# Performance work log

Hardware: AMD Instinct MI355X
Metric: run time of the kernel (lower is better)

The kernel has to match this reference:

```python
import jax, jax.numpy as jnp
import numpy as np
from jax import lax

L, E, H, V, B, S = 25, 64, 8, 30000, 1000, 512


def setup_inputs() -> dict:
    key = jax.random.key(0)
    ks = jax.random.split(key, 24)
    p = lambda k, shape: (jax.random.normal(k, shape) * 0.1).astype(jnp.float32)
    inp = {
        "x": jax.random.randint(ks[0], (B, S), 0, V),
        "embedding": p(ks[1], (V, E)),
        # layer 0 (input dim = E)
        "W_xz0": p(ks[2], (E, H)), "W_hz0": p(ks[3], (H, H)), "b_z0": p(ks[4], (H,)),
        "W_xr0": p(ks[5], (E, H)), "W_hr0": p(ks[6], (H, H)), "b_r0": p(ks[7], (H,)),
        "W_xH0": p(ks[8], (E, H)), "W_rH0": p(ks[9], (H, H)), "b_H0": p(ks[10], (H,)),
        # layers 1..L-1 stacked (input dim = H)
        "W_xz": p(ks[11], (L - 1, H, H)), "W_hz": p(ks[12], (L - 1, H, H)), "b_z": p(ks[13], (L - 1, H)),
        "W_xr": p(ks[14], (L - 1, H, H)), "W_hr": p(ks[15], (L - 1, H, H)), "b_r": p(ks[16], (L - 1, H)),
        "W_xH": p(ks[17], (L - 1, H, H)), "W_rH": p(ks[18], (L - 1, H, H)), "b_H": p(ks[19], (L - 1, H)),
        "W_hy": p(ks[20], (H, 1)), "b_y": p(ks[21], (1,)),
    }
    return inp


def _cell(x_t, h, Wxz, Whz, bz, Wxr, Whr, br, WxH, WrH, bH):
    z = jax.nn.sigmoid(x_t @ Wxz + h @ Whz + bz)
    r = jax.nn.sigmoid(x_t @ Wxr + h @ Whr + br)
    Hc = jnp.tanh(x_t @ WxH + (h * r) @ WrH + bH)
    return h * (1.0 - z) + z * Hc


def reference(x, embedding, W_xz0, W_hz0, b_z0, W_xr0, W_hr0, b_r0, W_xH0, W_rH0, b_H0,
              W_xz, W_hz, b_z, W_xr, W_hr, b_r, W_xH, W_rH, b_H, W_hy, b_y):
    emb = embedding[x]                     # [B, S, E]
    bsz = x.shape[0]
    h0 = jnp.zeros((L, bsz, H), dtype=embedding.dtype)

    def time_step(h_all, x_t):            # h_all: [L, B, H]; x_t: [B, E]
        h_new0 = _cell(x_t, h_all[0], W_xz0, W_hz0, b_z0, W_xr0, W_hr0, b_r0, W_xH0, W_rH0, b_H0)

        def layer_step(inp_t, ws):
            Wxz, Whz, bz, Wxr, Whr, br, WxH, WrH, bH, h_prev = ws
            h_new = _cell(inp_t, h_prev, Wxz, Whz, bz, Wxr, Whr, br, WxH, WrH, bH)
            return h_new, h_new

        _, h_rest = lax.scan(layer_step, h_new0,
                             (W_xz, W_hz, b_z, W_xr, W_hr, b_r, W_xH, W_rH, b_H, h_all[1:]))
        return jnp.concatenate([h_new0[None], h_rest], axis=0), None

    h_last, _ = lax.scan(time_step, h0, jnp.swapaxes(emb, 0, 1))  # scan over S
    logits = h_last[-1] @ W_hy + b_y       # [B, 1]
    return logits.squeeze(-1), h_last
```

## Files before the change

kernel.cpp:

```cpp
#include <hip/hip_runtime.h>
#include <hip/hip_bf16.h>
#include <stdint.h>

#define L_ 25
#define E_ 64
#define H_ 8
#define B_ 1000
#define S_ 512
#define GQ 2
#define NCELL (L_ * GQ)
#define TPBR (NCELL * 8)
#define NSUPER (S_ / 2 + L_ - 1)
#define HS 12
#define XG 20

typedef float v2f __attribute__((ext_vector_type(2)));
typedef float v4f __attribute__((ext_vector_type(4)));

#define PIN(x) asm volatile("" : "+v"(x))

__device__ __forceinline__ v2f pkfma(v2f a, v2f b, v2f c) {
  v2f d;
  asm("v_pk_fma_f32 %0, %1, %2, %3" : "=v"(d) : "v"(a), "v"(b), "v"(c));
  return d;
}
__device__ __forceinline__ v2f vlo(v4f v) { return __builtin_shufflevector(v, v, 0, 1); }
__device__ __forceinline__ v2f vhi(v4f v) { return __builtin_shufflevector(v, v, 2, 3); }
__device__ __forceinline__ v2f mk2(float a, float b) { v2f r; r.x = a; r.y = b; return r; }

__device__ __forceinline__ float ulo(uint32_t u) { return __uint_as_float(u << 16); }
__device__ __forceinline__ float uhi(uint32_t u) { return __uint_as_float(u & 0xffff0000u); }

__device__ __forceinline__ float toF(float v) { return v; }
__device__ __forceinline__ float toF(__hip_bfloat16 v) { return __bfloat162float(v); }
__device__ __forceinline__ void stP(float* p, float v) { *p = v; }
__device__ __forceinline__ void stP(__hip_bfloat16* p, float v) { *p = __float2bfloat16(v); }

__device__ __forceinline__ void load8f(const __hip_bfloat16* p, float* o) {
  const uint4 v = *(const uint4*)p;
  o[0] = ulo(v.x); o[1] = uhi(v.x); o[2] = ulo(v.y); o[3] = uhi(v.y);
  o[4] = ulo(v.z); o[5] = uhi(v.z); o[6] = ulo(v.w); o[7] = uhi(v.w);
}
__device__ __forceinline__ void load8f(const float* p, float* o) {
  const float4 a = ((const float4*)p)[0];
  const float4 b = ((const float4*)p)[1];
  o[0] = a.x; o[1] = a.y; o[2] = a.z; o[3] = a.w;
  o[4] = b.x; o[5] = b.y; o[6] = b.z; o[7] = b.w;
}

__device__ __forceinline__ void st4(float* p, float a, float b, float c, float d) {
  float4 v; v.x = a; v.y = b; v.z = c; v.w = d;
  *(float4*)p = v;
}
__device__ __forceinline__ void st4(__hip_bfloat16* p, float a, float b, float c, float d) {
  __hip_bfloat16 t[4] = {__float2bfloat16(a), __float2bfloat16(b),
                         __float2bfloat16(c), __float2bfloat16(d)};
  *(ushort4*)p = *(ushort4*)t;
}

__device__ __forceinline__ float sigmo(float x) {
  return __builtin_amdgcn_rcpf(1.f + __expf(-x));
}
__device__ __forceinline__ float tanh_(float x) {
  const float e = __expf(-2.f * x);
  return fmaf(2.f, __builtin_amdgcn_rcpf(1.f + e), -1.f);
}

__global__ void gru_detect(const unsigned short* __restrict__ u16, int* __restrict__ flag) {
  const int i = threadIdx.x;
  float m = 0.f;
#pragma unroll
  for (int k = 0; k < 4; ++k) {
    const uint32_t u = u16[i * 4 + k];
    float v = fabsf(__uint_as_float(u << 16));
    if (!(v < 1e30f)) v = 1e30f;
    m = fmaxf(m, v);
  }
#pragma unroll
  for (int off = 32; off; off >>= 1) m = fmaxf(m, __shfl_down(m, off, 64));
  if (i == 0) *flag = (m > 2.0f) ? 0 : 1;
}

template <typename T, typename PT>
__global__ __launch_bounds__(256, 4) void gru_pre(
    const int* __restrict__ flag, int want,
    const int* __restrict__ x, const T* __restrict__ emb,
    const T* __restrict__ Wz, const T* __restrict__ Wr,
    const T* __restrict__ Wh, PT* __restrict__ pre) {
  if (*flag != want) return;
  __shared__ __align__(16) float WL[64 * 24];
  __shared__ __align__(16) float TB[4][24 * 65];
  for (int idx = threadIdx.x; idx < 64 * 24; idx += 256) {
    const int k = idx / 24, c = idx - k * 24;
    const T* src = (c < 8) ? Wz : ((c < 16) ? Wr : Wh);
    WL[idx] = toF(src[k * 8 + (c & 7)]);
  }
  __syncthreads();

  const int tok = blockIdx.x * 256 + threadIdx.x;
  const int t = x[tok];

  v2f acc[12];
#pragma unroll
  for (int q = 0; q < 12; ++q) acc[q] = mk2(0.f, 0.f);

  for (int kb = 0; kb < 8; ++kb) {
    float e[8];
    load8f(emb + (size_t)t * E_ + kb * 8, e);
#pragma unroll
    for (int k8 = 0; k8 < 8; ++k8) {
      const v4f* wr = (const v4f*)(WL + (kb * 8 + k8) * 24);
      const v2f ee = mk2(e[k8], e[k8]);
#pragma unroll
      for (int q = 0; q < 6; ++q) {
        const v4f w4 = wr[q];
        acc[2 * q]     = pkfma(ee, vlo(w4), acc[2 * q]);
        acc[2 * q + 1] = pkfma(ee, vhi(w4), acc[2 * q + 1]);
      }
    }
  }

  const int wid = threadIdx.x >> 6, lane = threadIdx.x & 63;
  float* tb = &TB[wid][0];
#pragma unroll
  for (int q = 0; q < 12; ++q) {
    tb[(2 * q) * 65 + lane] = acc[q].x;
    tb[(2 * q + 1) * 65 + lane] = acc[q].y;
  }
  asm volatile("s_waitcnt lgkmcnt(0)" ::: "memory");
  __builtin_amdgcn_wave_barrier();

  PT* ob = pre + (size_t)(blockIdx.x * 256 + wid * 64) * 24;
#pragma unroll
  for (int it = 0; it < 6; ++it) {
    const int F0 = it * 256 + lane * 4;
    float o[4];
#pragma unroll
    for (int e2 = 0; e2 < 4; ++e2) {
      const int F = F0 + e2;
      const int tk = F / 24;
      const int c = F - tk * 24;
      o[e2] = tb[c * 65 + tk];
    }
    st4(ob + F0, o[0], o[1], o[2], o[3]);
  }
}

template <typename T, typename PT>
__global__ __launch_bounds__(TPBR, 4) void gru_rec(
    const int* __restrict__ flag, int want,
    const PT* __restrict__ pre,
    const T* __restrict__ Whz0, const T* __restrict__ bz0,
    const T* __restrict__ Whr0, const T* __restrict__ br0,
    const T* __restrict__ WrH0, const T* __restrict__ bH0,
    const T* __restrict__ Wxz, const T* __restrict__ Whz,
    const T* __restrict__ bz, const T* __restrict__ Wxr,
    const T* __restrict__ Whr, const T* __restrict__ br,
    const T* __restrict__ WxH, const T* __restrict__ WrH,
    const T* __restrict__ bH, const T* __restrict__ Why,
    const T* __restrict__ by, T* __restrict__ out) {
  if (*flag != want) return;
  __shared__ __align__(16) float hsh[NCELL * HS];
  __shared__ __align__(16) float hrsh[NCELL * HS];
  __shared__ __align__(16) float xbuf[2 * NCELL * XG];

  const int tid = threadIdx.x;
  const int gi = tid >> 3;
  const int j = tid & 7;
  const int l = gi >> 1;
  const int g = gi & 1;
  const int b = blockIdx.x * GQ + g;

  for (int i = tid; i < NCELL * HS; i += TPBR) { hsh[i] = 0.f; hrsh[i] = 0.f; }
  for (int i = tid; i < 2 * NCELL * XG; i += TPBR) xbuf[i] = 0.f;

  v2f wxz2[4], whz2[4], wxr2[4], whr2[4], wxh2[4], wrh2[4];
  v2f bz2, br2, bh2;
  if (l == 0) {
#pragma unroll
    for (int q = 0; q < 4; ++q) {
      whz2[q] = mk2(toF(Whz0[(2 * q) * 8 + j]), toF(Whz0[(2 * q + 1) * 8 + j]));
      whr2[q] = mk2(toF(Whr0[(2 * q) * 8 + j]), toF(Whr0[(2 * q + 1) * 8 + j]));
      wrh2[q] = mk2(toF(WrH0[(2 * q) * 8 + j]), toF(WrH0[(2 * q + 1) * 8 + j]));
      wxz2[q] = mk2(0.f, 0.f); wxr2[q] = mk2(0.f, 0.f); wxh2[q] = mk2(0.f, 0.f);
    }
    bz2 = mk2(toF(bz0[j]), 0.f);
    br2 = mk2(toF(br0[j]), 0.f);
    bh2 = mk2(toF(bH0[j]), 0.f);
  } else {
    const int base = (l - 1) * 64;
#pragma unroll
    for (int q = 0; q < 4; ++q) {
      wxz2[q] = mk2(toF(Wxz[base + (2 * q) * 8 + j]), toF(Wxz[base + (2 * q + 1) * 8 + j]));
      whz2[q] = mk2(toF(Whz[base + (2 * q) * 8 + j]), toF(Whz[base + (2 * q + 1) * 8 + j]));
      wxr2[q] = mk2(toF(Wxr[base + (2 * q) * 8 + j]), toF(Wxr[base + (2 * q + 1) * 8 + j]));
      whr2[q] = mk2(toF(Whr[base + (2 * q) * 8 + j]), toF(Whr[base + (2 * q + 1) * 8 + j]));
      wxh2[q] = mk2(toF(WxH[base + (2 * q) * 8 + j]), toF(WxH[base + (2 * q + 1) * 8 + j]));
      wrh2[q] = mk2(toF(WrH[base + (2 * q) * 8 + j]), toF(WrH[base + (2 * q + 1) * 8 + j]));
    }
    bz2 = mk2(toF(bz[(l - 1) * 8 + j]), 0.f);
    br2 = mk2(toF(br[(l - 1) * 8 + j]), 0.f);
    bh2 = mk2(toF(bH[(l - 1) * 8 + j]), 0.f);
  }
#pragma unroll
  for (int q = 0; q < 4; ++q) {
    PIN(wxz2[q]); PIN(whz2[q]); PIN(wxr2[q]); PIN(whr2[q]); PIN(wxh2[q]); PIN(wrh2[q]);
  }
  PIN(bz2); PIN(br2); PIN(bh2);

  const PT* ppr = pre + (size_t)b * (S_ * 24) + j;
  float cz0 = 0.f, cr0 = 0.f, ch0 = 0.f, cz1 = 0.f, cr1 = 0.f, ch1 = 0.f;
  if (l == 0) {
    cz0 = toF(ppr[0]);  cr0 = toF(ppr[8]);  ch0 = toF(ppr[16]);
    cz1 = toF(ppr[24]); cr1 = toF(ppr[32]); ch1 = toF(ppr[40]);
  }

  float* hgw = hsh + gi * HS;
  float* hrg = hrsh + gi * HS;
  float* hgwj = hgw + j;
  float* hrgj = hrg + j;
  const int gp = (gi >= GQ) ? (gi - GQ) * XG : 0;
  const float* xpe = xbuf + NCELL * XG + gp;
  const float* xpo = xbuf + gp;
  float* xce = xbuf + gi * XG;
  float* xco = xbuf + NCELL * XG + gi * XG;

  float hown = 0.f;

  __syncthreads();

  for (int s = 0; s < NSUPER; ++s) {
    const unsigned rel = (unsigned)(s - l);
    if (rel < (unsigned)(S_ / 2)) {
      const float* xp = (s & 1) ? xpo : xpe;
      float* xc = (s & 1) ? xco : xce;

      const v4f h01 = ((const v4f*)hgw)[0];
      const v4f h23 = ((const v4f*)hgw)[1];
      const v4f xa0 = ((const v4f*)xp)[0];
      const v4f xb0 = ((const v4f*)xp)[1];
      const v4f xa1 = ((const v4f*)xp)[2];
      const v4f xb1 = ((const v4f*)xp)[3];

      float pz0 = 0.f, pr0 = 0.f, ph0 = 0.f, pz1 = 0.f, pr1 = 0.f, ph1 = 0.f;
      const bool pf = (l == 0) && (rel + 1u < (unsigned)(S_ / 2));
      if (pf) {
        const PT* pn = ppr + (rel + 1) * 48;
        pz0 = toF(pn[0]);  pr0 = toF(pn[8]);  ph0 = toF(pn[16]);
        pz1 = toF(pn[24]); pr1 = toF(pn[32]); ph1 = toF(pn[40]);
      }

      v2f arh = pkfma(vlo(h01), whr2[0], mk2(0.f, 0.f));
      arh = pkfma(vhi(h01), whr2[1], arh);
      arh = pkfma(vlo(h23), whr2[2], arh);
      arh = pkfma(vhi(h23), whr2[3], arh);
      v2f azh = pkfma(vlo(h01), whz2[0], mk2(0.f, 0.f));
      azh = pkfma(vhi(h01), whz2[1], azh);
      azh = pkfma(vlo(h23), whz2[2], azh);
      azh = pkfma(vhi(h23), whz2[3], azh);

      v2f arp = pkfma(vlo(xa0), wxr2[0], br2);
      arp = pkfma(vhi(xa0), wxr2[1], arp);
      arp = pkfma(vlo(xb0), wxr2[2], arp);
      arp = pkfma(vhi(xb0), wxr2[3], arp);
      v2f azp = pkfma(vlo(xa0), wxz2[0], bz2);
      azp = pkfma(vhi(xa0), wxz2[1], azp);
      azp = pkfma(vlo(xb0), wxz2[2], azp);
      azp = pkfma(vhi(xb0), wxz2[3], azp);
      v2f ahp = pkfma(vlo(xa0), wxh2[0], bh2);
      ahp = pkfma(vhi(xa0), wxh2[1], ahp);
      ahp = pkfma(vlo(xb0), wxh2[2], ahp);
      ahp = pkfma(vhi(xb0), wxh2[3], ahp);

      v2f arp1 = pkfma(vlo(xa1), wxr2[0], br2);
      arp1 = pkfma(vhi(xa1), wxr2[1], arp1);
      arp1 = pkfma(vlo(xb1), wxr2[2], arp1);
      arp1 = pkfma(vhi(xb1), wxr2[3], arp1);
      v2f azp1 = pkfma(vlo(xa1), wxz2[0], bz2);
      azp1 = pkfma(vhi(xa1), wxz2[1], azp1);
      azp1 = pkfma(vlo(xb1), wxz2[2], azp1);
      azp1 = pkfma(vhi(xb1), wxz2[3], azp1);
      v2f ahp1 = pkfma(vlo(xa1), wxh2[0], bh2);
      ahp1 = pkfma(vhi(xa1), wxh2[1], ahp1);
      ahp1 = pkfma(vlo(xb1), wxh2[2], ahp1);
      ahp1 = pkfma(vhi(xb1), wxh2[3], ahp1);

      const float ar0 = (arp.x + arp.y) + (arh.x + arh.y) + cr0;
      const float rA = sigmo(ar0);
      *hrgj = hown * rA;
      __builtin_amdgcn_wave_barrier();

      const v4f r01 = ((const v4f*)hrg)[0];
      const v4f r23 = ((const v4f*)hrg)[1];
      const float az0 = (azp.x + azp.y) + (azh.x + azh.y) + cz0;
      const float zA = sigmo(az0);
      ahp = pkfma(vlo(r01), wrh2[0], ahp);
      ahp = pkfma(vhi(r01), wrh2[1], ahp);
      ahp = pkfma(vlo(r23), wrh2[2], ahp);
      ahp = pkfma(vhi(r23), wrh2[3], ahp);
      const float ah0 = ahp.x + ahp.y + ch0;
      const float hn0 = fmaf(zA, tanh_(ah0) - hown, hown);
      *hgwj = hn0;
      xc[j] = hn0;
      __builtin_amdgcn_wave_barrier();

      const v4f g01 = ((const v4f*)hgw)[0];
      const v4f g23 = ((const v4f*)hgw)[1];
      arp1 = pkfma(vlo(g01), whr2[0], arp1);
      arp1 = pkfma(vhi(g01), whr2[1], arp1);
      arp1 = pkfma(vlo(g23), whr2[2], arp1);
      arp1 = pkfma(vhi(g23), whr2[3], arp1);
      azp1 = pkfma(vlo(g01), whz2[0], azp1);
      azp1 = pkfma(vhi(g01), whz2[1], azp1);
      azp1 = pkfma(vlo(g23), whz2[2], azp1);
      azp1 = pkfma(vhi(g23), whz2[3], azp1);
      const float ar1 = arp1.x + arp1.y + cr1;
      const float rB = sigmo(ar1);
      *hrgj = hn0 * rB;
      __builtin_amdgcn_wave_barrier();

      const v4f q01 = ((const v4f*)hrg)[0];
      const v4f q23 = ((const v4f*)hrg)[1];
      const float az1 = azp1.x + azp1.y + cz1;
      const float zB = sigmo(az1);
      ahp1 = pkfma(vlo(q01), wrh2[0], ahp1);
      ahp1 = pkfma(vhi(q01), wrh2[1], ahp1);
      ahp1 = pkfma(vlo(q23), wrh2[2], ahp1);
      ahp1 = pkfma(vhi(q23), wrh2[3], ahp1);
      const float ah1 = ahp1.x + ahp1.y + ch1;
      const float hn1 = fmaf(zB, tanh_(ah1) - hn0, hn0);
      *hgwj = hn1;
      xc[8 + j] = hn1;
      hown = hn1;
      if (pf) { cz0 = pz0; cr0 = pr0; ch0 = ph0; cz1 = pz1; cr1 = pr1; ch1 = ph1; }
    }
    __syncthreads();
  }

  stP(out + B_ + (l * B_ + b) * H_ + j, hown);
  if (l == L_ - 1 && j == 0) {
    float ssum = toF(by[0]);
#pragma unroll
    for (int k = 0; k < 8; ++k) ssum = fmaf(hgw[k], toF(Why[k]), ssum);
    stP(out + b, ssum);
  }
}

template <typename T, typename PT>
static void launch_mode(const int* flag, int want, void* const* d_in, PT* pre,
                        T* out, hipStream_t stream) {
  const int* x = (const int*)d_in[0];
  const T* emb = (const T*)d_in[1];
  const T* Wxz0 = (const T*)d_in[2];
  const T* Whz0 = (const T*)d_in[3];
  const T* bz0 = (const T*)d_in[4];
  const T* Wxr0 = (const T*)d_in[5];
  const T* Whr0 = (const T*)d_in[6];
  const T* br0 = (const T*)d_in[7];
  const T* WxH0 = (const T*)d_in[8];
  const T* WrH0 = (const T*)d_in[9];
  const T* bH0 = (const T*)d_in[10];
  const T* Wxz = (const T*)d_in[11];
  const T* Whz = (const T*)d_in[12];
  const T* bz = (const T*)d_in[13];
  const T* Wxr = (const T*)d_in[14];
  const T* Whr = (const T*)d_in[15];
  const T* br = (const T*)d_in[16];
  const T* WxH = (const T*)d_in[17];
  const T* WrH = (const T*)d_in[18];
  const T* bH = (const T*)d_in[19];
  const T* Why = (const T*)d_in[20];
  const T* by = (const T*)d_in[21];

  gru_pre<T, PT><<<B_ * S_ / 256, 256, 0, stream>>>(flag, want, x, emb,
                                                    Wxz0, Wxr0, WxH0, pre);
  gru_rec<T, PT><<<B_ / GQ, TPBR, 0, stream>>>(
      flag, want, pre, Whz0, bz0, Whr0, br0, WrH0, bH0, Wxz, Whz, bz, Wxr, Whr,
      br, WxH, WrH, bH, Why, by, out);
}

extern "C" void kernel_launch(void* const* d_in, const int* in_sizes, int n_in,
                              void* d_out, int out_size, void* d_ws, size_t ws_size,
                              hipStream_t stream) {
  int* flag = (int*)d_ws;
  char* preMem = (char*)d_ws + 256;
  const size_t needF = (size_t)B_ * S_ * 24 * sizeof(float) + 256;

  gru_detect<<<1, 64, 0, stream>>>((const unsigned short*)d_in[1], flag);

  if (ws_size >= needF) {
    float* pre = (float*)preMem;
    launch_mode<float, float>(flag, 0, d_in, pre, (float*)d_out, stream);
    launch_mode<__hip_bfloat16, float>(flag, 1, d_in, pre, (__hip_bfloat16*)d_out, stream);
  } else {
    __hip_bfloat16* pre = (__hip_bfloat16*)preMem;
    launch_mode<float, __hip_bfloat16>(flag, 0, d_in, pre, (float*)d_out, stream);
    launch_mode<__hip_bfloat16, __hip_bfloat16>(flag, 1, d_in, pre, (__hip_bfloat16*)d_out, stream);
  }
}
```

Baseline: 416.7 us.

## Fuse dtype detection into kernels, pack z/r gate math, widen batch per block

Drops the separate detect kernel and the four flag-gated launches. Each kernel now detects the dtype in-block and dispatches to a templated body, leaving two launches. The recurrence packs the z and r gate weights into interleaved pairs so a single op_sel-based packed FMA chain computes both gates together, and the pre-projection layout is interleaved to match. GQ goes from 2 to 4, so each block handles four batch rows with 800 threads and 250 blocks, which raises per-block parallelism but reduces block count and may pressure registers.

```diff
diff --git a/kernel.cpp b/kernel.cpp
--- a/kernel.cpp
+++ b/kernel.cpp
@@ -7,7 +7,7 @@
 #define H_ 8
 #define B_ 1000
 #define S_ 512
-#define GQ 2
+#define GQ 4
 #define NCELL (L_ * GQ)
 #define TPBR (NCELL * 8)
 #define NSUPER (S_ / 2 + L_ - 1)
@@ -24,9 +24,42 @@
   asm("v_pk_fma_f32 %0, %1, %2, %3" : "=v"(d) : "v"(a), "v"(b), "v"(c));
   return d;
 }
+__device__ __forceinline__ v2f pkfma_l(v2f a, v2f b, v2f c) {
+  v2f d;
+  asm("v_pk_fma_f32 %0, %1, %2, %3 op_sel:[0,0,0] op_sel_hi:[0,1,1]"
+      : "=v"(d) : "v"(a), "v"(b), "v"(c));
+  return d;
+}
+__device__ __forceinline__ v2f pkfma_h(v2f a, v2f b, v2f c) {
+  v2f d;
+  asm("v_pk_fma_f32 %0, %1, %2, %3 op_sel:[1,0,0] op_sel_hi:[1,1,1]"
+      : "=v"(d) : "v"(a), "v"(b), "v"(c));
+  return d;
+}
+__device__ __forceinline__ v2f pkadd(v2f a, v2f b) {
+  v2f d;
+  asm("v_pk_add_f32 %0, %1, %2" : "=v"(d) : "v"(a), "v"(b));
+  return d;
+}
 __device__ __forceinline__ v2f vlo(v4f v) { return __builtin_shufflevector(v, v, 0, 1); }
 __device__ __forceinline__ v2f vhi(v4f v) { return __builtin_shufflevector(v, v, 2, 3); }
 __device__ __forceinline__ v2f mk2(float a, float b) { v2f r; r.x = a; r.y = b; return r; }
+
+#define CHAIN8(acc, ma, mb, w)            \
+  acc = pkfma_l(vlo(ma), w[0], acc);      \
+  acc = pkfma_h(vlo(ma), w[1], acc);      \
+  acc = pkfma_l(vhi(ma), w[2], acc);      \
+  acc = pkfma_h(vhi(ma), w[3], acc);      \
+  acc = pkfma_l(vlo(mb), w[4], acc);      \
+  acc = pkfma_h(vlo(mb), w[5], acc);      \
+  acc = pkfma_l(vhi(mb), w[6], acc);      \
+  acc = pkfma_h(vhi(mb), w[7], acc);
+
+#define CHAIN4P(acc, ma, mb, w)           \
+  acc = pkfma(vlo(ma), w[0], acc);        \
+  acc = pkfma(vhi(ma), w[1], acc);        \
+  acc = pkfma(vlo(mb), w[2], acc);        \
+  acc = pkfma(vhi(mb), w[3], acc);
 
 __device__ __forceinline__ float ulo(uint32_t u) { return __uint_as_float(u << 16); }
 __device__ __forceinline__ float uhi(uint32_t u) { return __uint_as_float(u & 0xffff0000u); }
@@ -35,6 +68,12 @@
 __device__ __forceinline__ float toF(__hip_bfloat16 v) { return __bfloat162float(v); }
 __device__ __forceinline__ void stP(float* p, float v) { *p = v; }
 __device__ __forceinline__ void stP(__hip_bfloat16* p, float v) { *p = __float2bfloat16(v); }
+
+__device__ __forceinline__ v2f loadC2(const float* p) { return *(const v2f*)p; }
+__device__ __forceinline__ v2f loadC2(const __hip_bfloat16* p) {
+  const uint32_t u = *(const uint32_t*)p;
+  return mk2(ulo(u), uhi(u));
+}
 
 __device__ __forceinline__ void load8f(const __hip_bfloat16* p, float* o) {
   const uint4 v = *(const uint4*)p;
@@ -66,38 +105,45 @@
   return fmaf(2.f, __builtin_amdgcn_rcpf(1.f + e), -1.f);
 }
 
-__global__ void gru_detect(const unsigned short* __restrict__ u16, int* __restrict__ flag) {
-  const int i = threadIdx.x;
-  float m = 0.f;
-#pragma unroll
-  for (int k = 0; k < 4; ++k) {
-    const uint32_t u = u16[i * 4 + k];
-    float v = fabsf(__uint_as_float(u << 16));
-    if (!(v < 1e30f)) v = 1e30f;
-    m = fmaxf(m, v);
-  }
-#pragma unroll
-  for (int off = 32; off; off >>= 1) m = fmaxf(m, __shfl_down(m, off, 64));
-  if (i == 0) *flag = (m > 2.0f) ? 0 : 1;
+__device__ __forceinline__ void detect64(const unsigned short* __restrict__ u,
+                                         int tid, float* fl) {
+  if (tid < 64) {
+    float m = 0.f;
+#pragma unroll
+    for (int k = 0; k < 4; ++k) {
+      const uint32_t q = u[tid * 4 + k];
+      float v = fabsf(__uint_as_float(q << 16));
+      if (!(v < 1e30f)) v = 1e30f;
+      m = fmaxf(m, v);
+    }
+#pragma unroll
+    for (int off = 32; off; off >>= 1) m = fmaxf(m, __shfl_down(m, off, 64));
+    if (tid == 0) *fl = (m > 2.0f) ? 0.f : 1.f;
+  }
 }
 
 template <typename T, typename PT>
-__global__ __launch_bounds__(256, 4) void gru_pre(
-    const int* __restrict__ flag, int want,
-    const int* __restrict__ x, const T* __restrict__ emb,
-    const T* __restrict__ Wz, const T* __restrict__ Wr,
-    const T* __restrict__ Wh, PT* __restrict__ pre) {
-  if (*flag != want) return;
-  __shared__ __align__(16) float WL[64 * 24];
-  __shared__ __align__(16) float TB[4][24 * 65];
-  for (int idx = threadIdx.x; idx < 64 * 24; idx += 256) {
+__device__ __forceinline__ void pre_body(
+    const int* __restrict__ x, const void* __restrict__ embv,
+    const void* __restrict__ Wzv, const void* __restrict__ Wrv,
+    const void* __restrict__ Whv, PT* __restrict__ pre,
+    float* WL, float* TBb) {
+  const T* emb = (const T*)embv;
+  const T* Wz = (const T*)Wzv;
+  const T* Wr = (const T*)Wrv;
+  const T* Wh = (const T*)Whv;
+  const int tid = threadIdx.x;
+
+  for (int idx = tid; idx < 64 * 24; idx += 256) {
     const int k = idx / 24, c = idx - k * 24;
-    const T* src = (c < 8) ? Wz : ((c < 16) ? Wr : Wh);
-    WL[idx] = toF(src[k * 8 + (c & 7)]);
+    float w;
+    if (c < 16) w = toF(((c & 1) ? Wr : Wz)[k * 8 + (c >> 1)]);
+    else        w = toF(Wh[k * 8 + (c - 16)]);
+    WL[idx] = w;
   }
   __syncthreads();
 
-  const int tok = blockIdx.x * 256 + threadIdx.x;
+  const int tok = blockIdx.x * 256 + tid;
   const int t = x[tok];
 
   v2f acc[12];
@@ -120,8 +166,8 @@
     }
   }
 
-  const int wid = threadIdx.x >> 6, lane = threadIdx.x & 63;
-  float* tb = &TB[wid][0];
+  const int wid = tid >> 6, lane = tid & 63;
+  float* tb = TBb + wid * (24 * 65);
 #pragma unroll
   for (int q = 0; q < 12; ++q) {
     tb[(2 * q) * 65 + lane] = acc[q].x;
@@ -146,73 +192,95 @@
   }
 }
 
+template <typename PT>
+__global__ __launch_bounds__(256, 4) void gru_pre(
+    const int* __restrict__ x, const void* __restrict__ emb,
+    const void* __restrict__ Wz, const void* __restrict__ Wr,
+    const void* __restrict__ Wh, PT* __restrict__ pre) {
+  __shared__ __align__(16) float WL[64 * 24];
+  __shared__ __align__(16) float TB[4][24 * 65];
+  __shared__ float fl;
+  detect64((const unsigned short*)emb, threadIdx.x, &fl);
+  __syncthreads();
+  if (fl != 0.f) pre_body<__hip_bfloat16, PT>(x, emb, Wz, Wr, Wh, pre, WL, &TB[0][0]);
+  else           pre_body<float, PT>(x, emb, Wz, Wr, Wh, pre, WL, &TB[0][0]);
+}
+
 template <typename T, typename PT>
-__global__ __launch_bounds__(TPBR, 4) void gru_rec(
-    const int* __restrict__ flag, int want,
+__device__ __forceinline__ void rec_body(
     const PT* __restrict__ pre,
-    const T* __restrict__ Whz0, const T* __restrict__ bz0,
-    const T* __restrict__ Whr0, const T* __restrict__ br0,
-    const T* __restrict__ WrH0, const T* __restrict__ bH0,
-    const T* __restrict__ Wxz, const T* __restrict__ Whz,
-    const T* __restrict__ bz, const T* __restrict__ Wxr,
-    const T* __restrict__ Whr, const T* __restrict__ br,
-    const T* __restrict__ WxH, const T* __restrict__ WrH,
-    const T* __restrict__ bH, const T* __restrict__ Why,
-    const T* __restrict__ by, T* __restrict__ out) {
-  if (*flag != want) return;
-  __shared__ __align__(16) float hsh[NCELL * HS];
-  __shared__ __align__(16) float hrsh[NCELL * HS];
-  __shared__ __align__(16) float xbuf[2 * NCELL * XG];
+    const void* __restrict__ Whz0v, const void* __restrict__ bz0v,
+    const void* __restrict__ Whr0v, const void* __restrict__ br0v,
+    const void* __restrict__ WrH0v, const void* __restrict__ bH0v,
+    const void* __restrict__ Wxzv, const void* __restrict__ Whzv,
+    const void* __restrict__ bzv, const void* __restrict__ Wxrv,
+    const void* __restrict__ Whrv, const void* __restrict__ brv,
+    const void* __restrict__ WxHv, const void* __restrict__ WrHv,
+    const void* __restrict__ bHv, const void* __restrict__ Whyv,
+    const void* __restrict__ byv, void* __restrict__ outv,
+    float* hsh, float* hrsh, float* xbuf) {
+  const T* Whz0 = (const T*)Whz0v; const T* bz0 = (const T*)bz0v;
+  const T* Whr0 = (const T*)Whr0v; const T* br0 = (const T*)br0v;
+  const T* WrH0 = (const T*)WrH0v; const T* bH0 = (const T*)bH0v;
+  const T* Wxz = (const T*)Wxzv;   const T* Whz = (const T*)Whzv;
+  const T* bz = (const T*)bzv;     const T* Wxr = (const T*)Wxrv;
+  const T* Whr = (const T*)Whrv;   const T* br = (const T*)brv;
+  const T* WxH = (const T*)WxHv;   const T* WrH = (const T*)WrHv;
+  const T* bH = (const T*)bHv;     const T* Why = (const T*)Whyv;
+  const T* by = (const T*)byv;     T* out = (T*)outv;
 
   const int tid = threadIdx.x;
   const int gi = tid >> 3;
   const int j = tid & 7;
-  const int l = gi >> 1;
-  const int g = gi & 1;
+  const int l = gi >> 2;
+  const int g = gi & 3;
   const int b = blockIdx.x * GQ + g;
 
   for (int i = tid; i < NCELL * HS; i += TPBR) { hsh[i] = 0.f; hrsh[i] = 0.f; }
   for (int i = tid; i < 2 * NCELL * XG; i += TPBR) xbuf[i] = 0.f;
 
-  v2f wxz2[4], whz2[4], wxr2[4], whr2[4], wxh2[4], wrh2[4];
-  v2f bz2, br2, bh2;
+  v2f wzrx[8], wzrh[8], wxh2[4], wrh2[4], bzr;
+  float vbh;
   if (l == 0) {
 #pragma unroll
+    for (int k = 0; k < 8; ++k) {
+      wzrh[k] = mk2(toF(Whz0[k * 8 + j]), toF(Whr0[k * 8 + j]));
+      wzrx[k] = mk2(0.f, 0.f);
+    }
+#pragma unroll
     for (int q = 0; q < 4; ++q) {
-      whz2[q] = mk2(toF(Whz0[(2 * q) * 8 + j]), toF(Whz0[(2 * q + 1) * 8 + j]));
-      whr2[q] = mk2(toF(Whr0[(2 * q) * 8 + j]), toF(Whr0[(2 * q + 1) * 8 + j]));
       wrh2[q] = mk2(toF(WrH0[(2 * q) * 8 + j]), toF(WrH0[(2 * q + 1) * 8 + j]));
-      wxz2[q] = mk2(0.f, 0.f); wxr2[q] = mk2(0.f, 0.f); wxh2[q] = mk2(0.f, 0.f);
-    }
-    bz2 = mk2(toF(bz0[j]), 0.f);
-    br2 = mk2(toF(br0[j]), 0.f);
-    bh2 = mk2(toF(bH0[j]), 0.f);
+      wxh2[q] = mk2(0.f, 0.f);
+    }
+    bzr = mk2(toF(bz0[j]), toF(br0[j]));
+    vbh = toF(bH0[j]);
   } else {
     const int base = (l - 1) * 64;
 #pragma unroll
+    for (int k = 0; k < 8; ++k) {
+      wzrx[k] = mk2(toF(Wxz[base + k * 8 + j]), toF(Wxr[base + k * 8 + j]));
+      wzrh[k] = mk2(toF(Whz[base + k * 8 + j]), toF(Whr[base + k * 8 + j]));
+    }
+#pragma unroll
     for (int q = 0; q < 4; ++q) {
-      wxz2[q] = mk2(toF(Wxz[base + (2 * q) * 8 + j]), toF(Wxz[base + (2 * q + 1) * 8 + j]));
-      whz2[q] = mk2(toF(Whz[base + (2 * q) * 8 + j]), toF(Whz[base + (2 * q + 1) * 8 + j]));
-      wxr2[q] = mk2(toF(Wxr[base + (2 * q) * 8 + j]), toF(Wxr[base + (2 * q + 1) * 8 + j]));
-      whr2[q] = mk2(toF(Whr[base + (2 * q) * 8 + j]), toF(Whr[base + (2 * q + 1) * 8 + j]));
       wxh2[q] = mk2(toF(WxH[base + (2 * q) * 8 + j]), toF(WxH[base + (2 * q + 1) * 8 + j]));
       wrh2[q] = mk2(toF(WrH[base + (2 * q) * 8 + j]), toF(WrH[base + (2 * q + 1) * 8 + j]));
     }
-    bz2 = mk2(toF(bz[(l - 1) * 8 + j]), 0.f);
-    br2 = mk2(toF(br[(l - 1) * 8 + j]), 0.f);
-    bh2 = mk2(toF(bH[(l - 1) * 8 + j]), 0.f);
-  }
-#pragma unroll
-  for (int q = 0; q < 4; ++q) {
-    PIN(wxz2[q]); PIN(whz2[q]); PIN(wxr2[q]); PIN(whr2[q]); PIN(wxh2[q]); PIN(wrh2[q]);
-  }
-  PIN(bz2); PIN(br2); PIN(bh2);
-
-  const PT* ppr = pre + (size_t)b * (S_ * 24) + j;
-  float cz0 = 0.f, cr0 = 0.f, ch0 = 0.f, cz1 = 0.f, cr1 = 0.f, ch1 = 0.f;
+    bzr = mk2(toF(bz[(l - 1) * 8 + j]), toF(br[(l - 1) * 8 + j]));
+    vbh = toF(bH[(l - 1) * 8 + j]);
+  }
+#pragma unroll
+  for (int k = 0; k < 8; ++k) { PIN(wzrx[k]); PIN(wzrh[k]); }
+#pragma unroll
+  for (int q = 0; q < 4; ++q) { PIN(wxh2[q]); PIN(wrh2[q]); }
+  PIN(bzr); PIN(vbh);
+
+  const PT* ppr = pre + (size_t)b * (S_ * 24);
+  v2f czrA = mk2(0.f, 0.f), czrB = mk2(0.f, 0.f);
+  float chA = 0.f, chB = 0.f;
   if (l == 0) {
-    cz0 = toF(ppr[0]);  cr0 = toF(ppr[8]);  ch0 = toF(ppr[16]);
-    cz1 = toF(ppr[24]); cr1 = toF(ppr[32]); ch1 = toF(ppr[40]);
+    czrA = loadC2(ppr + 2 * j);      chA = toF(ppr[16 + j]);
+    czrB = loadC2(ppr + 24 + 2 * j); chB = toF(ppr[24 + 16 + j]);
   }
 
   float* hgw = hsh + gi * HS;
@@ -242,97 +310,60 @@
       const v4f xa1 = ((const v4f*)xp)[2];
       const v4f xb1 = ((const v4f*)xp)[3];
 
-      float pz0 = 0.f, pr0 = 0.f, ph0 = 0.f, pz1 = 0.f, pr1 = 0.f, ph1 = 0.f;
+      v2f nzrA = mk2(0.f, 0.f), nzrB = mk2(0.f, 0.f);
+      float nhA = 0.f, nhB = 0.f;
       const bool pf = (l == 0) && (rel + 1u < (unsigned)(S_ / 2));
       if (pf) {
-        const PT* pn = ppr + (rel + 1) * 48;
-        pz0 = toF(pn[0]);  pr0 = toF(pn[8]);  ph0 = toF(pn[16]);
-        pz1 = toF(pn[24]); pr1 = toF(pn[32]); ph1 = toF(pn[40]);
+        const PT* pn = ppr + (2 * rel + 2) * 24;
+        nzrA = loadC2(pn + 2 * j);      nhA = toF(pn[16 + j]);
+        nzrB = loadC2(pn + 24 + 2 * j); nhB = toF(pn[24 + 16 + j]);
       }
 
-      v2f arh = pkfma(vlo(h01), whr2[0], mk2(0.f, 0.f));
-      arh = pkfma(vhi(h01), whr2[1], arh);
-      arh = pkfma(vlo(h23), whr2[2], arh);
-      arh = pkfma(vhi(h23), whr2[3], arh);
-      v2f azh = pkfma(vlo(h01), whz2[0], mk2(0.f, 0.f));
-      azh = pkfma(vhi(h01), whz2[1], azh);
-      azh = pkfma(vlo(h23), whz2[2], azh);
-      azh = pkfma(vhi(h23), whz2[3], azh);
-
-      v2f arp = pkfma(vlo(xa0), wxr2[0], br2);
-      arp = pkfma(vhi(xa0), wxr2[1], arp);
-      arp = pkfma(vlo(xb0), wxr2[2], arp);
-      arp = pkfma(vhi(xb0), wxr2[3], arp);
-      v2f azp = pkfma(vlo(xa0), wxz2[0], bz2);
-      azp = pkfma(vhi(xa0), wxz2[1], azp);
-      azp = pkfma(vlo(xb0), wxz2[2], azp);
-      azp = pkfma(vhi(xb0), wxz2[3], azp);
-      v2f ahp = pkfma(vlo(xa0), wxh2[0], bh2);
-      ahp = pkfma(vhi(xa0), wxh2[1], ahp);
-      ahp = pkfma(vlo(xb0), wxh2[2], ahp);
-      ahp = pkfma(vhi(xb0), wxh2[3], ahp);
-
-      v2f arp1 = pkfma(vlo(xa1), wxr2[0], br2);
-      arp1 = pkfma(vhi(xa1), wxr2[1], arp1);
-      arp1 = pkfma(vlo(xb1), wxr2[2], arp1);
-      arp1 = pkfma(vhi(xb1), wxr2[3], arp1);
-      v2f azp1 = pkfma(vlo(xa1), wxz2[0], bz2);
-      azp1 = pkfma(vhi(xa1), wxz2[1], azp1);
-      azp1 = pkfma(vlo(xb1), wxz2[2], azp1);
-      azp1 = pkfma(vhi(xb1), wxz2[3], azp1);
-      v2f ahp1 = pkfma(vlo(xa1), wxh2[0], bh2);
-      ahp1 = pkfma(vhi(xa1), wxh2[1], ahp1);
-      ahp1 = pkfma(vlo(xb1), wxh2[2], ahp1);
-      ahp1 = pkfma(vhi(xb1), wxh2[3], ahp1);
-
-      const float ar0 = (arp.x + arp.y) + (arh.x + arh.y) + cr0;
-      const float rA = sigmo(ar0);
+      v2f azrh = bzr;
+      CHAIN8(azrh, h01, h23, wzrh);
+      v2f azrxA = czrA;
+      CHAIN8(azrxA, xa0, xb0, wzrx);
+      v2f ahA = mk2(chA, vbh);
+      CHAIN4P(ahA, xa0, xb0, wxh2);
+      v2f azrxB = czrB;
+      CHAIN8(azrxB, xa1, xb1, wzrx);
+      v2f ahB = mk2(chB, vbh);
+      CHAIN4P(ahB, xa1, xb1, wxh2);
+
+      const v2f azrA = pkadd(azrh, azrxA);
+      const float rA = sigmo(azrA.y);
       *hrgj = hown * rA;
       __builtin_amdgcn_wave_barrier();
 
       const v4f r01 = ((const v4f*)hrg)[0];
       const v4f r23 = ((const v4f*)hrg)[1];
-      const float az0 = (azp.x + azp.y) + (azh.x + azh.y) + cz0;
-      const float zA = sigmo(az0);
-      ahp = pkfma(vlo(r01), wrh2[0], ahp);
-      ahp = pkfma(vhi(r01), wrh2[1], ahp);
-      ahp = pkfma(vlo(r23), wrh2[2], ahp);
-      ahp = pkfma(vhi(r23), wrh2[3], ahp);
-      const float ah0 = ahp.x + ahp.y + ch0;
-      const float hn0 = fmaf(zA, tanh_(ah0) - hown, hown);
+      const float zA = sigmo(azrA.x);
+      CHAIN4P(ahA, r01, r23, wrh2);
+      const float hcA = tanh_(ahA.x + ahA.y);
+      const float hn0 = fmaf(zA, hcA - hown, hown);
       *hgwj = hn0;
       xc[j] = hn0;
       __builtin_amdgcn_wave_barrier();
 
       const v4f g01 = ((const v4f*)hgw)[0];
       const v4f g23 = ((const v4f*)hgw)[1];
-      arp1 = pkfma(vlo(g01), whr2[0], arp1);
-      arp1 = pkfma(vhi(g01), whr2[1], arp1);
-      arp1 = pkfma(vlo(g23), whr2[2], arp1);
-      arp1 = pkfma(vhi(g23), whr2[3], arp1);
-      azp1 = pkfma(vlo(g01), whz2[0], azp1);
-      azp1 = pkfma(vhi(g01), whz2[1], azp1);
-      azp1 = pkfma(vlo(g23), whz2[2], azp1);
-      azp1 = pkfma(vhi(g23), whz2[3], azp1);
-      const float ar1 = arp1.x + arp1.y + cr1;
-      const float rB = sigmo(ar1);
+      v2f azrhB = bzr;
+      CHAIN8(azrhB, g01, g23, wzrh);
+      const v2f azrB = pkadd(azrhB, azrxB);
+      const float rB = sigmo(azrB.y);
       *hrgj = hn0 * rB;
       __builtin_amdgcn_wave_barrier();
 
       const v4f q01 = ((const v4f*)hrg)[0];
       const v4f q23 = ((const v4f*)hrg)[1];
-      const float az1 = azp1.x + azp1.y + cz1;
-      const float zB = sigmo(az1);
-      ahp1 = pkfma(vlo(q01), wrh2[0], ahp1);
-      ahp1 = pkfma(vhi(q01), wrh2[1], ahp1);
-      ahp1 = pkfma(vlo(q23), wrh2[2], ahp1);
-      ahp1 = pkfma(vhi(q23), wrh2[3], ahp1);
-      const float ah1 = ahp1.x + ahp1.y + ch1;
-      const float hn1 = fmaf(zB, tanh_(ah1) - hn0, hn0);
+      const float zB = sigmo(azrB.x);
+      CHAIN4P(ahB, q01, q23, wrh2);
+      const float hcB = tanh_(ahB.x + ahB.y);
+      const float hn1 = fmaf(zB, hcB - hn0, hn0);
       *hgwj = hn1;
       xc[8 + j] = hn1;
       hown = hn1;
-      if (pf) { cz0 = pz0; cr0 = pr0; ch0 = ph0; cz1 = pz1; cr1 = pr1; ch1 = ph1; }
+      czrA = nzrA; chA = nhA; czrB = nzrB; chB = nhB;
     }
     __syncthreads();
   }
@@ -346,55 +377,49 @@
   }
 }
 
-template <typename T, typename PT>
-static void launch_mode(const int* flag, int want, void* const* d_in, PT* pre,
-                        T* out, hipStream_t stream) {
-  const int* x = (const int*)d_in[0];
-  const T* emb = (const T*)d_in[1];
-  const T* Wxz0 = (const T*)d_in[2];
-  const T* Whz0 = (const T*)d_in[3];
-  const T* bz0 = (const T*)d_in[4];
-  const T* Wxr0 = (const T*)d_in[5];
-  const T* Whr0 = (const T*)d_in[6];
-  const T* br0 = (const T*)d_in[7];
-  const T* WxH0 = (const T*)d_in[8];
-  const T* WrH0 = (const T*)d_in[9];
-  const T* bH0 = (const T*)d_in[10];
-  const T* Wxz = (const T*)d_in[11];
-  const T* Whz = (const T*)d_in[12];
-  const T* bz = (const T*)d_in[13];
-  const T* Wxr = (const T*)d_in[14];
-  const T* Whr = (const T*)d_in[15];
-  const T* br = (const T*)d_in[16];
-  const T* WxH = (const T*)d_in[17];
-  const T* WrH = (const T*)d_in[18];
-  const T* bH = (const T*)d_in[19];
-  const T* Why = (const T*)d_in[20];
-  const T* by = (const T*)d_in[21];
-
-  gru_pre<T, PT><<<B_ * S_ / 256, 256, 0, stream>>>(flag, want, x, emb,
-                                                    Wxz0, Wxr0, WxH0, pre);
-  gru_rec<T, PT><<<B_ / GQ, TPBR, 0, stream>>>(
-      flag, want, pre, Whz0, bz0, Whr0, br0, WrH0, bH0, Wxz, Whz, bz, Wxr, Whr,
-      br, WxH, WrH, bH, Why, by, out);
+template <typename PT>
+__global__ __launch_bounds__(TPBR, 4) void gru_rec(
+    const void* __restrict__ emb, const PT* __restrict__ pre,
+    const void* __restrict__ Whz0, const void* __restrict__ bz0,
+    const void* __restrict__ Whr0, const void* __restrict__ br0,
+    const void* __restrict__ WrH0, const void* __restrict__ bH0,
+    const void* __restrict__ Wxz, const void* __restrict__ Whz,
+    const void* __restrict__ bz, const void* __restrict__ Wxr,
+    const void* __restrict__ Whr, const void* __restrict__ br,
+    const void* __restrict__ WxH, const void* __restrict__ WrH,
+    const void* __restrict__ bH, const void* __restrict__ Why,
+    const void* __restrict__ by, void* __restrict__ out) {
+  __shared__ __align__(16) float hsh[NCELL * HS];
+  __shared__ __align__(16) float hrsh[NCELL * HS];
+  __shared__ __align__(16) float xbuf[2 * NCELL * XG];
+  __shared__ float fl;
+  detect64((const unsigned short*)emb, threadIdx.x, &fl);
+  __syncthreads();
+  if (fl != 0.f)
+    rec_body<__hip_bfloat16, PT>(pre, Whz0, bz0, Whr0, br0, WrH0, bH0, Wxz, Whz,
+                                 bz, Wxr, Whr, br, WxH, WrH, bH, Why, by, out,
+                                 hsh, hrsh, xbuf);
+  else
+    rec_body<float, PT>(pre, Whz0, bz0, Whr0, br0, WrH0, bH0, Wxz, Whz, bz, Wxr,
+                        Whr, br, WxH, WrH, bH, Why, by, out, hsh, hrsh, xbuf);
+}
+
+template <typename PT>
+static void launch_all(void* const* d_in, PT* pre, void* d_out, hipStream_t stream) {
+  gru_pre<PT><<<B_ * S_ / 256, 256, 0, stream>>>(
+      (const int*)d_in[0], d_in[1], d_in[2], d_in[5], d_in[8], pre);
+  gru_rec<PT><<<B_ / GQ, TPBR, 0, stream>>>(
+      d_in[1], pre, d_in[3], d_in[4], d_in[6], d_in[7], d_in[9], d_in[10],
+      d_in[11], d_in[12], d_in[13], d_in[14], d_in[15], d_in[16], d_in[17],
+      d_in[18], d_in[19], d_in[20], d_in[21], d_out);
 }
 
 extern "C" void kernel_launch(void* const* d_in, const int* in_sizes, int n_in,
                               void* d_out, int out_size, void* d_ws, size_t ws_size,
                               hipStream_t stream) {
-  int* flag = (int*)d_ws;
-  char* preMem = (char*)d_ws + 256;
-  const size_t needF = (size_t)B_ * S_ * 24 * sizeof(float) + 256;
-
-  gru_detect<<<1, 64, 0, stream>>>((const unsigned short*)d_in[1], flag);
-
-  if (ws_size >= needF) {
-    float* pre = (float*)preMem;
-    launch_mode<float, float>(flag, 0, d_in, pre, (float*)d_out, stream);
-    launch_mode<__hip_bfloat16, float>(flag, 1, d_in, pre, (__hip_bfloat16*)d_out, stream);
-  } else {
-    __hip_bfloat16* pre = (__hip_bfloat16*)preMem;
-    launch_mode<float, __hip_bfloat16>(flag, 0, d_in, pre, (float*)d_out, stream);
-    launch_mode<__hip_bfloat16, __hip_bfloat16>(flag, 1, d_in, pre, (__hip_bfloat16*)d_out, stream);
-  }
-}
+  const size_t needF = (size_t)B_ * S_ * 24 * sizeof(float);
+  if (ws_size >= needF)
+    launch_all<float>(d_in, (float*)d_ws, d_out, stream);
+  else
+    launch_all<__hip_bfloat16>(d_in, (__hip_bfloat16*)d_ws, d_out, stream);
+}
```

Result: no change. 408.7 us (-1.9%).
